# Kernel tuning notes

Hardware: AMD Instinct MI355X
Metric: run time of the kernel (lower is better)

Reference implementation:

```python
import jax, jax.numpy as jnp
import numpy as np
import math

N, S, T, D = 4, 2048, 2048, 1024

def setup_inputs() -> dict:
    key = jax.random.key(0)
    ks = jax.random.split(key, 6)
    scale = 1.0 / math.sqrt(D)
    return {
        "query": jax.random.normal(ks[0], (N, S, D), dtype=jnp.float32),
        "key": jax.random.normal(ks[1], (N, T, D), dtype=jnp.float32),
        "value": jax.random.normal(ks[2], (N, T, D), dtype=jnp.float32),
        # causal mask: 1 = attend, 0 = masked out (masked_fill where mask == 0)
        "attn_mask": jnp.tril(jnp.ones((S, T), dtype=jnp.int32)),
        "Wq": jax.random.normal(ks[3], (D, D), dtype=jnp.float32) * scale,
        "Wk": jax.random.normal(ks[4], (D, D), dtype=jnp.float32) * scale,
        "Wv": jax.random.normal(ks[5], (D, D), dtype=jnp.float32) * scale,
    }

def reference(query, key, value, attn_mask, Wq, Wk, Wv):
    # nn.Linear(bias=False): y = x @ W.T
    q = jnp.einsum('nsd,ed->nse', query, Wq)
    k = jnp.einsum('ntd,ed->nte', key, Wk)
    v = jnp.einsum('ntd,ed->nte', value, Wv)
    # scaled dot-product scores [N, S, T]
    dot = jnp.einsum('nse,nte->nst', q, k) / jnp.sqrt(jnp.asarray(D, q.dtype))
    dot = jnp.where(attn_mask == 0, -jnp.inf, dot)
    scores = jax.nn.softmax(dot, axis=-1)
    # dropout is identity in eval mode
    y = jnp.einsum('nst,nte->nse', scores, v)
    return y
```

## Files before the change

### kernel.cpp

```cpp
#include <hip/hip_runtime.h>
#include <math.h>

using u16 = unsigned short;
typedef __attribute__((ext_vector_type(8))) __bf16 bf16x8;
typedef __attribute__((ext_vector_type(4))) float f32x4;
typedef __attribute__((ext_vector_type(4))) float f4v;
typedef __attribute__((ext_vector_type(8))) u16 u16x8;

__device__ __forceinline__ u16 f2bf(float f) {
  unsigned u = __float_as_uint(f);
  u += 0x7fffu + ((u >> 16) & 1u);
  return (u16)(u >> 16);
}
__device__ __forceinline__ float bf2f(u16 b) {
  unsigned u = ((unsigned)b) << 16;
  return __uint_as_float(u);
}

__device__ __forceinline__ void gload16(const void* g, void* l) {
  __builtin_amdgcn_global_load_lds(
      (const __attribute__((address_space(1))) unsigned int*)g,
      (__attribute__((address_space(3))) unsigned int*)l, 16, 0, 0);
}

__device__ __forceinline__ f32x4 MF(bf16x8 a, bf16x8 b, f32x4 c) {
  return __builtin_amdgcn_mfma_f32_16x16x32_bf16(a, b, c, 0, 0, 0);
}

__global__ __launch_bounds__(256) void cast3_f32_bf16(
    const float* __restrict__ p0, const float* __restrict__ p1,
    const float* __restrict__ p2, u16* __restrict__ out, size_t ostride) {
  int z = blockIdx.z;
  const float* in = (z == 0) ? p0 : (z == 1) ? p1 : p2;
  size_t i = ((size_t)blockIdx.x * 256 + threadIdx.x) * 8;
  f4v a = *reinterpret_cast<const f4v*>(in + i);
  f4v b = *reinterpret_cast<const f4v*>(in + i + 4);
  u16x8 r;
  r[0] = f2bf(a[0]); r[1] = f2bf(a[1]); r[2] = f2bf(a[2]); r[3] = f2bf(a[3]);
  r[4] = f2bf(b[0]); r[5] = f2bf(b[1]); r[6] = f2bf(b[2]); r[7] = f2bf(b[3]);
  *reinterpret_cast<u16x8*>(out + z * ostride + i) = r;
}

__global__ __launch_bounds__(256) void transpose_bf16k(const u16* __restrict__ in,
                                                       u16* __restrict__ out) {
  __shared__ u16 t[64][65];
  int c0 = blockIdx.x * 64, r0 = blockIdx.y * 64;
  size_t zb = (size_t)blockIdx.z * 2048 * 1024;
  const u16* I = in + zb;
  u16* O = out + zb;
  int tx = threadIdx.x & 63, ty = threadIdx.x >> 6;
  #pragma unroll
  for (int i = 0; i < 64; i += 4)
    t[ty + i][tx] = I[(size_t)(r0 + ty + i) * 1024 + c0 + tx];
  __syncthreads();
  #pragma unroll
  for (int i = 0; i < 64; i += 4)
    O[(size_t)(c0 + ty + i) * 2048 + r0 + tx] = t[tx][ty + i];
}

template<typename OutT, int MODE>
__global__ __launch_bounds__(512) void gemm_bt8(
    const u16* __restrict__ A, const u16* __restrict__ B, OutT* __restrict__ C,
    int K, int lda, int ldb, int ldc,
    size_t sA, size_t sB, size_t sC, float alpha,
    OutT* __restrict__ C1, OutT* __restrict__ C2) {
  int bn, bm, bz = 0;
  int kEnd = K;
  const u16 *Ag, *Bg;
  OutT* Cg;
  if (MODE == 1) {
    int h = blockIdx.x;
    int l = (h & 7) * 68 + (h >> 3);
    bz = l / 136;
    int t = l % 136;
    bm = (int)((sqrtf(8.f * (float)t + 1.f) - 1.f) * 0.5f);
    while ((bm + 1) * (bm + 2) / 2 <= t) ++bm;
    while (bm * (bm + 1) / 2 > t) --bm;
    bn = t - bm * (bm + 1) / 2;
    Ag = A + sA * bz + (size_t)bm * 128 * lda;
    Bg = B + sB * bz + (size_t)bn * 128 * ldb;
    Cg = C + sC * bz;
  } else if (MODE == 2) {
    int l = blockIdx.x;
    bm = 15 - (l >> 5);
    int rest = l & 31;
    bz = rest >> 3;
    bn = rest & 7;
    kEnd = (K < (bm + 1) * 128) ? K : (bm + 1) * 128;
    Ag = A + sA * bz + (size_t)bm * 128 * lda;
    Bg = B + sB * bz + (size_t)bn * 128 * ldb;
    Cg = C + sC * bz;
  } else {
    int h = blockIdx.x;
    int l = (h & 7) * 192 + (h >> 3);
    bn = l & 7;
    int bm192 = l >> 3;
    int which = bm192 >> 6;
    bm = bm192 & 63;
    Ag = A + (size_t)bm192 * 128 * lda;
    Bg = B + (size_t)which * sB + (size_t)bn * 128 * ldb;
    Cg = (which == 0) ? C : (which == 1) ? C1 : C2;
  }

  __shared__ __align__(16) u16 As[2][128 * 32];
  __shared__ __align__(16) u16 Bs[2][128 * 32];

  const int tid = threadIdx.x;
  const int lane = tid & 63, wv = tid >> 6;
  const int wr = wv >> 2, wc = wv & 3;
  const int fr = lane & 15, kq = (lane >> 4) * 8;

  const int e0 = wv * 512 + lane * 8;
  const int r0 = e0 >> 5, c0 = e0 & 31;
  const u16* a0 = Ag + (size_t)r0 * lda + c0;
  const u16* b0 = Bg + (size_t)r0 * ldb + c0;

  f32x4 acc[4][2] = {};
  const int nt = kEnd / 32;

  gload16(a0, &As[0][wv * 512]);
  gload16(b0, &Bs[0][wv * 512]);
  __syncthreads();

  for (int t = 0; t < nt; ++t) {
    const int cur = t & 1;
    if (t + 1 < nt) {
      const int k0 = (t + 1) * 32;
      gload16(a0 + k0, &As[cur ^ 1][wv * 512]);
      gload16(b0 + k0, &Bs[cur ^ 1][wv * 512]);
    }
    bf16x8 af[4], bfv[2];
    #pragma unroll
    for (int m = 0; m < 4; ++m)
      af[m] = *reinterpret_cast<const bf16x8*>(&As[cur][(wr * 64 + m * 16 + fr) * 32 + kq]);
    #pragma unroll
    for (int n = 0; n < 2; ++n)
      bfv[n] = *reinterpret_cast<const bf16x8*>(&Bs[cur][(wc * 32 + n * 16 + fr) * 32 + kq]);
    #pragma unroll
    for (int m = 0; m < 4; ++m)
      #pragma unroll
      for (int n = 0; n < 2; ++n)
        acc[m][n] = MF(af[m], bfv[n], acc[m][n]);
    __syncthreads();
  }

  const int row0 = bm * 128 + wr * 64 + (lane >> 4) * 4;
  const int col0 = bn * 128 + wc * 32 + fr;
  #pragma unroll
  for (int m = 0; m < 4; ++m)
    #pragma unroll
    for (int n = 0; n < 2; ++n) {
      #pragma unroll
      for (int j = 0; j < 4; ++j) {
        float val = acc[m][n][j] * alpha;
        size_t idx = (size_t)(row0 + m * 16 + j) * ldc + (col0 + n * 16);
        if constexpr (sizeof(OutT) == 2) Cg[idx] = f2bf(val);
        else Cg[idx] = val;
      }
    }
}

__global__ __launch_bounds__(256) void softmax_causal(u16* __restrict__ sc) {
  int r = blockIdx.x;
  int s = r & 2047;
  u16* row = sc + (size_t)r * 2048;
  int tid = threadIdx.x;
  int t0 = tid * 8;
  u16x8 raw = {0, 0, 0, 0, 0, 0, 0, 0};
  if (t0 <= s) raw = *reinterpret_cast<const u16x8*>(row + t0);
  float v[8];
  float mx = -1e30f;
  #pragma unroll
  for (int j = 0; j < 8; ++j) {
    v[j] = ((t0 + j) <= s) ? bf2f(raw[j]) : -1e30f;
    mx = fmaxf(mx, v[j]);
  }
  #pragma unroll
  for (int o = 32; o; o >>= 1) mx = fmaxf(mx, __shfl_xor(mx, o, 64));
  __shared__ float red[8];
  if ((tid & 63) == 0) red[tid >> 6] = mx;
  __syncthreads();
  mx = fmaxf(fmaxf(red[0], red[1]), fmaxf(red[2], red[3]));
  float p[8];
  float sum = 0.f;
  #pragma unroll
  for (int j = 0; j < 8; ++j) {
    p[j] = ((t0 + j) <= s) ? __expf(v[j] - mx) : 0.f;
    sum += p[j];
  }
  #pragma unroll
  for (int o = 32; o; o >>= 1) sum += __shfl_xor(sum, o, 64);
  if ((tid & 63) == 0) red[4 + (tid >> 6)] = sum;
  __syncthreads();
  sum = red[4] + red[5] + red[6] + red[7];
  float inv = 1.0f / sum;
  u16x8 o8;
  #pragma unroll
  for (int j = 0; j < 8; ++j) o8[j] = f2bf(p[j] * inv);
  if (t0 <= (s | 127))
    *reinterpret_cast<u16x8*>(row + t0) = o8;
}

extern "C" void kernel_launch(void* const* d_in, const int* in_sizes, int n_in,
                              void* d_out, int out_size, void* d_ws, size_t ws_size,
                              hipStream_t stream) {
  const float* q  = (const float*)d_in[0];
  const float* k  = (const float*)d_in[1];
  const float* v  = (const float*)d_in[2];
  const float* Wq = (const float*)d_in[4];
  const float* Wk = (const float*)d_in[5];
  const float* Wv = (const float*)d_in[6];
  float* out = (float*)d_out;
  char* ws = (char*)d_ws;

  const size_t MB = 1024ull * 1024ull;
  u16* sc   = (u16*)ws;
  u16* qb   = (u16*)(ws + 0 * MB);
  u16* wqb  = (u16*)(ws + 48 * MB);
  u16* Vp   = (u16*)(ws + 54 * MB);
  u16* Vt   = (u16*)(ws + 70 * MB);
  u16* Kp   = (u16*)(ws + 86 * MB);
  u16* Qp   = (u16*)(ws + 102 * MB);
  (void)in_sizes; (void)n_in; (void)out_size; (void)ws_size;

  cast3_f32_bf16<<<dim3(4096, 1, 3), 256, 0, stream>>>(q, k, v, qb, 8ull * MB);
  cast3_f32_bf16<<<dim3(512, 1, 3), 256, 0, stream>>>(Wq, Wk, Wv, wqb, 1ull * MB);

  gemm_bt8<u16, 3><<<1536, 512, 0, stream>>>(
      qb, wqb, Qp, 1024, 1024, 1024, 1024,
      0, 1ull * MB, 0, 1.0f, Kp, Vp);

  transpose_bf16k<<<dim3(16, 32, 4), 256, 0, stream>>>(Vp, Vt);

  gemm_bt8<u16, 1><<<544, 512, 0, stream>>>(
      Qp, Kp, sc, 1024, 1024, 1024, 2048,
      (size_t)2048 * 1024, (size_t)2048 * 1024, (size_t)2048 * 2048, 0.03125f,
      nullptr, nullptr);

  softmax_causal<<<8192, 256, 0, stream>>>(sc);

  gemm_bt8<float, 2><<<512, 512, 0, stream>>>(
      sc, Vt, out, 2048, 2048, 2048, 1024,
      (size_t)2048 * 2048, (size_t)1024 * 2048, (size_t)2048 * 1024, 1.0f,
      nullptr, nullptr);
}
```

Baseline: 179.9 us.

## Fold Wk into query projection via precomputed Wq^T Wk product

Scores are rewritten as q·(Wq^T Wk)·k^T. A small 1024^3 GEMM builds the combined weight Wk^T-major product once, so the key projection GEMM is dropped and the raw bf16 key input is used directly in the score GEMM. This removes one of the three large projection GEMMs (8192x1024x1024) at the cost of an extra weight-transpose-cast kernel and a 64-block weight GEMM. The fused weight is stored in bf16, which adds an extra rounding step to the scores.

```diff
diff --git a/kernel.cpp b/kernel.cpp
--- a/kernel.cpp
+++ b/kernel.cpp
@@ -41,6 +41,24 @@
   *reinterpret_cast<u16x8*>(out + z * ostride + i) = r;
 }
 
+__global__ __launch_bounds__(256) void tcast_w(
+    const float* __restrict__ wk, const float* __restrict__ wq,
+    u16* __restrict__ wkT, u16* __restrict__ wqT) {
+  __shared__ float t[64][65];
+  int z = blockIdx.z;
+  const float* I = z ? wq : wk;
+  u16* O = z ? wqT : wkT;
+  int c0 = blockIdx.x * 64, r0 = blockIdx.y * 64;
+  int tx = threadIdx.x & 63, ty = threadIdx.x >> 6;
+  #pragma unroll
+  for (int i = 0; i < 64; i += 4)
+    t[ty + i][tx] = I[(size_t)(r0 + ty + i) * 1024 + c0 + tx];
+  __syncthreads();
+  #pragma unroll
+  for (int i = 0; i < 64; i += 4)
+    O[(size_t)(c0 + ty + i) * 1024 + r0 + tx] = f2bf(t[tx][ty + i]);
+}
+
 __global__ __launch_bounds__(256) void transpose_bf16k(const u16* __restrict__ in,
                                                        u16* __restrict__ out) {
   __shared__ u16 t[64][65];
@@ -63,12 +81,18 @@
     const u16* __restrict__ A, const u16* __restrict__ B, OutT* __restrict__ C,
     int K, int lda, int ldb, int ldc,
     size_t sA, size_t sB, size_t sC, float alpha,
-    OutT* __restrict__ C1, OutT* __restrict__ C2) {
+    OutT* __restrict__ C1) {
   int bn, bm, bz = 0;
   int kEnd = K;
   const u16 *Ag, *Bg;
   OutT* Cg;
-  if (MODE == 1) {
+  if (MODE == 0) {
+    bm = blockIdx.x >> 3;
+    bn = blockIdx.x & 7;
+    Ag = A + (size_t)bm * 128 * lda;
+    Bg = B + (size_t)bn * 128 * ldb;
+    Cg = C;
+  } else if (MODE == 1) {
     int h = blockIdx.x;
     int l = (h & 7) * 68 + (h >> 3);
     bz = l / 136;
@@ -92,14 +116,14 @@
     Cg = C + sC * bz;
   } else {
     int h = blockIdx.x;
-    int l = (h & 7) * 192 + (h >> 3);
+    int l = (h & 7) * 128 + (h >> 3);
     bn = l & 7;
-    int bm192 = l >> 3;
-    int which = bm192 >> 6;
-    bm = bm192 & 63;
-    Ag = A + (size_t)bm192 * 128 * lda;
+    int bm128 = l >> 3;
+    int which = bm128 >> 6;
+    bm = bm128 & 63;
+    Ag = A + (size_t)bm128 * 128 * lda;
     Bg = B + (size_t)which * sB + (size_t)bn * 128 * ldb;
-    Cg = (which == 0) ? C : (which == 1) ? C1 : C2;
+    Cg = (which == 0) ? C : C1;
   }
 
   __shared__ __align__(16) u16 As[2][128 * 32];
@@ -215,32 +239,40 @@
 
   const size_t MB = 1024ull * 1024ull;
   u16* sc   = (u16*)ws;
-  u16* qb   = (u16*)(ws + 0 * MB);
-  u16* wqb  = (u16*)(ws + 48 * MB);
-  u16* Vp   = (u16*)(ws + 54 * MB);
-  u16* Vt   = (u16*)(ws + 70 * MB);
-  u16* Kp   = (u16*)(ws + 86 * MB);
-  u16* Qp   = (u16*)(ws + 102 * MB);
+  u16* qb   = (u16*)ws;
+  u16* xk   = (u16*)(ws + 32 * MB);
+  u16* wsl  = (u16*)(ws + 48 * MB);
+  u16* wkT  = (u16*)(ws + 52 * MB);
+  u16* wqT  = (u16*)(ws + 54 * MB);
+  u16* Vp   = (u16*)(ws + 56 * MB);
+  u16* Vt   = (u16*)(ws + 72 * MB);
+  u16* Yq   = (u16*)(ws + 88 * MB);
   (void)in_sizes; (void)n_in; (void)out_size; (void)ws_size;
 
-  cast3_f32_bf16<<<dim3(4096, 1, 3), 256, 0, stream>>>(q, k, v, qb, 8ull * MB);
-  cast3_f32_bf16<<<dim3(512, 1, 3), 256, 0, stream>>>(Wq, Wk, Wv, wqb, 1ull * MB);
-
-  gemm_bt8<u16, 3><<<1536, 512, 0, stream>>>(
-      qb, wqb, Qp, 1024, 1024, 1024, 1024,
-      0, 1ull * MB, 0, 1.0f, Kp, Vp);
+  cast3_f32_bf16<<<dim3(4096, 1, 3), 256, 0, stream>>>(q, v, k, qb, 8ull * MB);
+
+  tcast_w<<<dim3(16, 16, 2), 256, 0, stream>>>(Wk, Wq, wkT, wqT);
+  cast3_f32_bf16<<<dim3(512, 1, 1), 256, 0, stream>>>(Wv, nullptr, nullptr,
+                                                      wsl + 1048576, 0);
+
+  gemm_bt8<u16, 0><<<64, 512, 0, stream>>>(
+      wkT, wqT, wsl, 1024, 1024, 1024, 1024, 0, 0, 0, 1.0f, nullptr);
+
+  gemm_bt8<u16, 3><<<1024, 512, 0, stream>>>(
+      qb, wsl, Yq, 1024, 1024, 1024, 1024,
+      0, 1ull * MB, 0, 1.0f, Vp);
 
   transpose_bf16k<<<dim3(16, 32, 4), 256, 0, stream>>>(Vp, Vt);
 
   gemm_bt8<u16, 1><<<544, 512, 0, stream>>>(
-      Qp, Kp, sc, 1024, 1024, 1024, 2048,
+      Yq, xk, sc, 1024, 1024, 1024, 2048,
       (size_t)2048 * 1024, (size_t)2048 * 1024, (size_t)2048 * 2048, 0.03125f,
-      nullptr, nullptr);
+      nullptr);
 
   softmax_causal<<<8192, 256, 0, stream>>>(sc);
 
   gemm_bt8<float, 2><<<512, 512, 0, stream>>>(
       sc, Vt, out, 2048, 2048, 2048, 1024,
       (size_t)2048 * 2048, (size_t)1024 * 2048, (size_t)2048 * 1024, 1.0f,
-      nullptr, nullptr);
-}
+      nullptr);
+}
```

Result: no change. 179.0 us (-0.5%).
